# Optimization experiments

Hardware: AMD Instinct MI355X
Metric: run time of the kernel (lower is better)

Reference implementation:

```python
import jax, jax.numpy as jnp
import numpy as np

N = 50000       # nodes per layer
L = 2           # multiplex layers
F_IN = 128
F_OUT = 32
E_L = 800000    # in-layer edges per layer
NEG_SLOPE = 0.2  # LeakyReLU(0.2)


def _merge_edges(edges_per_layer):
    # offset each layer's edges into the global L*N index space
    parts = [edges_per_layer[i] + i * N for i in range(L)]
    all_edges = jnp.concatenate(parts, axis=1)
    dt = all_edges.dtype
    # self loops on every (layer, node)
    self_loops = jnp.tile(jnp.arange(L * N, dtype=dt)[None, :], (2, 1))
    all_edges = jnp.concatenate([all_edges, self_loops], axis=1)
    # interlayer loops: torch.combinations(arange(L), r=2) + flip([0,1])
    pairs = np.array([(i, j) for i in range(L) for j in range(i + 1, L)], dtype=np.int64)
    pairs = np.concatenate([pairs, pairs[::-1, ::-1]], axis=0)
    all_nodes = np.arange(L * N, dtype=np.int64).reshape(L, N)
    src = all_nodes[pairs[:, 0]].reshape(-1)
    trg = all_nodes[pairs[:, 1]].reshape(-1)
    inter = jnp.asarray(np.stack([src, trg], axis=0)).astype(dt)
    return jnp.concatenate([all_edges, inter], axis=1)  # [2, E_total]


def setup_inputs() -> dict:
    key = jax.random.key(0)
    k1, k2, k3, k4, k5 = jax.random.split(key, 5)
    return {
        "x": jax.random.normal(k1, (1, N, F_IN), dtype=jnp.float32),
        "edge_index0": jax.random.randint(k2, (2, E_L), 0, N, dtype=jnp.int32),
        "edge_index1": jax.random.randint(k3, (2, E_L), 0, N, dtype=jnp.int32),
        "W_proj": jax.random.normal(k4, (L * F_OUT, F_IN), dtype=jnp.float32) * 0.05,
        "W_merge": jax.random.normal(k5, (F_OUT, L * F_OUT), dtype=jnp.float32) * 0.05,
        "bias": jnp.zeros((L, F_OUT), dtype=jnp.float32),
    }


def reference(x, edge_index0, edge_index1, W_proj, W_merge, bias):
    # dropout_prob=0 -> dropout is identity (eval-mode semantics)
    B = x.shape[0]
    edges = _merge_edges([edge_index0, edge_index1])
    src, trg = edges[0], edges[1]
    # degree normalization (naming follows original: in_deg from src, out_deg from trg)
    in_deg = 1.0 / jnp.sqrt(jnp.zeros(L * N, x.dtype).at[src].add(1.0))
    out_deg = 1.0 / jnp.sqrt(jnp.zeros(L * N, x.dtype).at[trg].add(1.0))
    # project F_IN -> L*F_OUT, then split features into L chunks concatenated on node dim
    proj = jnp.einsum('bnf,of->bno', x, W_proj)                 # [B, N, L*F_OUT]
    proj = proj.reshape(B, N, L, F_OUT).transpose(0, 2, 1, 3).reshape(B, L * N, F_OUT)
    proj = proj * out_deg[None, :, None]
    lifted = proj[:, src, :]                                    # [B, E, F_OUT] gather
    agg = jnp.zeros((B, L * N, F_OUT), x.dtype).at[:, trg, :].add(lifted)  # scatter_add
    agg = agg * in_deg[None, :, None]
    out = agg.reshape(B, L, N, F_OUT).transpose(0, 2, 1, 3)     # [B, N, L, F_OUT]
    out = jax.nn.leaky_relu(out + bias, NEG_SLOPE)
    return jnp.einsum('bnk,ok->bno', out.reshape(B, N, L * F_OUT), W_merge)  # [B, N, F_OUT]
```

## Files before the change

kernel.cpp:

```cpp
#include <hip/hip_runtime.h>

#define N_NODES 50000
#define F_IN 128
#define F_OUT 32
#define E_L 800000
#define NEG_SLOPE 0.2f
#define LN 100000
#define NE 1600000
#define BSH 6
#define BNODES 64
#define NB 782
#define CAP 2368
#define PBLOCKS 256
#define PCHUNK 6250

__global__ __launch_bounds__(512) void partition_kernel(
    const int* __restrict__ e0, const int* __restrict__ e1,
    int* __restrict__ cur_t, int* __restrict__ cur_s,
    int* __restrict__ trgbuf, unsigned char* __restrict__ srcbuf) {
    __shared__ int hist_t[NB], hist_s[NB], res_t[NB], res_s[NB];
    const int t = threadIdx.x, b = blockIdx.x;
    for (int i = t; i < NB; i += 512) { hist_t[i] = 0; hist_s[i] = 0; }
    __syncthreads();
    const int base = b * PCHUNK;
    for (int i = base + t; i < base + PCHUNK; i += 512) {
        const int l = (i >= E_L) ? 1 : 0;
        const int e = i - l * E_L;
        const int* ei = l ? e1 : e0;
        const int src = ei[e], trg = ei[E_L + e];
        atomicAdd(&hist_t[trg >> BSH], 1);
        atomicAdd(&hist_s[src >> BSH], 1);
    }
    __syncthreads();
    for (int i = t; i < NB; i += 512) {
        res_t[i] = hist_t[i] ? atomicAdd(&cur_t[i], hist_t[i]) : 0;
        res_s[i] = hist_s[i] ? atomicAdd(&cur_s[i], hist_s[i]) : 0;
    }
    __syncthreads();
    for (int i = t; i < NB; i += 512) { hist_t[i] = 0; hist_s[i] = 0; }
    __syncthreads();
    for (int i = base + t; i < base + PCHUNK; i += 512) {
        const int l = (i >= E_L) ? 1 : 0;
        const int e = i - l * E_L;
        const int* ei = l ? e1 : e0;
        const int src = ei[e], trg = ei[E_L + e];
        const int tb = trg >> BSH, sb = src >> BSH;
        const int st = res_t[tb] + atomicAdd(&hist_t[tb], 1);
        const int ss = res_s[sb] + atomicAdd(&hist_s[sb], 1);
        if (st < CAP)
            trgbuf[tb * CAP + st] =
                (((l << 6) | (trg & 63)) << 17) | (src + l * N_NODES);
        if (ss < CAP)
            srcbuf[sb * CAP + ss] = (unsigned char)((l << 6) | (src & 63));
    }
}

__global__ __launch_bounds__(256) void count_kernel(
    const int* __restrict__ cur_t, const int* __restrict__ cur_s,
    const int* __restrict__ trgbuf, const unsigned char* __restrict__ srcbuf,
    int* __restrict__ cnt_trg, int* __restrict__ cnt_src) {
    __shared__ int ht[128], hs[128];
    const int t = threadIdx.x, b = blockIdx.x;
    if (t < 128) { ht[t] = 0; hs[t] = 0; }
    __syncthreads();
    const int ct = min(cur_t[b], CAP), cs = min(cur_s[b], CAP);
    for (int i = t; i < ct; i += 256)
        atomicAdd(&ht[(trgbuf[b * CAP + i] >> 17) & 127], 1);
    for (int i = t; i < cs; i += 256)
        atomicAdd(&hs[srcbuf[b * CAP + i] & 127], 1);
    __syncthreads();
    if (t < 128) {
        const int l = t >> 6, n = b * BNODES + (t & 63);
        if (n < N_NODES) {
            cnt_trg[l * N_NODES + n] = ht[t];
            cnt_src[l * N_NODES + n] = hs[t];
        }
    }
}

__global__ __launch_bounds__(256) void proj_kernel(
    const float* __restrict__ x, const float* __restrict__ Wp,
    const int* __restrict__ cnt_trg, float* __restrict__ scaled) {
    __shared__ float Wtt[64][132];
    __shared__ float xt[8][F_IN];
    const int t = threadIdx.x;
    for (int i = t; i < 64 * F_IN; i += 256) {
        int o = i >> 7, k = i & 127;
        Wtt[o][k] = Wp[i];
    }
    const int lane = t & 63, w = t >> 6;
    const int ntiles = N_NODES / 8;
    for (int tile = blockIdx.x; tile < ntiles; tile += gridDim.x) {
        const int base = tile * 8;
        __syncthreads();
        ((float4*)&xt[0][0])[t] = ((const float4*)(x + (size_t)base * F_IN))[t];
        __syncthreads();
        const int n0 = w, n1 = w + 4;
        float acc0 = 0.f, acc1 = 0.f;
        #pragma unroll
        for (int k = 0; k < F_IN; k += 4) {
            float4 wv = *(const float4*)&Wtt[lane][k];
            float4 x0 = *(const float4*)&xt[n0][k];
            float4 x1 = *(const float4*)&xt[n1][k];
            acc0 += wv.x * x0.x + wv.y * x0.y + wv.z * x0.z + wv.w * x0.w;
            acc1 += wv.x * x1.x + wv.y * x1.y + wv.z * x1.z + wv.w * x1.w;
        }
        const int l = lane >> 5, f = lane & 31;
        {
            const int v = l * N_NODES + base + n0;
            const float od = 1.0f / sqrtf((float)(cnt_trg[v] + 2));
            scaled[(size_t)v * F_OUT + f] = acc0 * od;
        }
        {
            const int v = l * N_NODES + base + n1;
            const float od = 1.0f / sqrtf((float)(cnt_trg[v] + 2));
            scaled[(size_t)v * F_OUT + f] = acc1 * od;
        }
    }
}

__global__ __launch_bounds__(512) void mega_kernel(
    const int* __restrict__ cur_t, const int* __restrict__ trgbuf,
    const int* __restrict__ cnt_trg, const int* __restrict__ cnt_src,
    const float* __restrict__ scaled, const float* __restrict__ Wm,
    const float* __restrict__ bias, float* __restrict__ out) {
    __shared__ int   colx[CAP];
    __shared__ int   rp[128], rdeg[128], cursor[128], sc[128];
    __shared__ float h[BNODES][64];
    __shared__ float Wt[64][32];
    __shared__ float bs[64];
    const int t = threadIdx.x, b = blockIdx.x;
    for (int i = t; i < 2048; i += 512) Wt[i >> 5][i & 31] = Wm[(i & 31) * 64 + (i >> 5)];
    if (t < 64) bs[t] = bias[t];
    int cnt_r = 0;
    if (t < 128) {
        const int l = t >> 6, n = b * BNODES + (t & 63);
        cnt_r = (n < N_NODES) ? cnt_trg[l * N_NODES + n] : 0;
        rdeg[t] = cnt_r; sc[t] = cnt_r;
    }
    __syncthreads();
    for (int off = 1; off < 128; off <<= 1) {
        int add = (t < 128 && t >= off) ? sc[t - off] : 0;
        __syncthreads();
        if (t < 128) sc[t] += add;
        __syncthreads();
    }
    if (t < 128) { rp[t] = sc[t] - cnt_r; cursor[t] = sc[t] - cnt_r; }
    __syncthreads();
    const int total = min(cur_t[b], CAP);
    for (int i = t; i < total; i += 512) {
        const int p = trgbuf[b * CAP + i];
        const int slot = atomicAdd(&cursor[(p >> 17) & 127], 1);
        colx[slot] = p & 0x1FFFF;
    }
    __syncthreads();
    const int grp = t >> 3, f = (t & 7) * 4;
    #pragma unroll
    for (int rr0 = 0; rr0 < 2; ++rr0) {
        const int rr = grp + rr0 * 64;
        const int l = rr >> 6, nl = rr & 63, n = b * BNODES + nl;
        if (n < N_NODES) {
            const int s0 = rp[rr], d = rdeg[rr];
            float4 acc = make_float4(0.f, 0.f, 0.f, 0.f);
            #pragma unroll 4
            for (int i = 0; i < d; ++i) {
                const int u = colx[s0 + i];
                const float4 g = *(const float4*)(scaled + (size_t)u * F_OUT + f);
                acc.x += g.x; acc.y += g.y; acc.z += g.z; acc.w += g.w;
            }
            const int v = l * N_NODES + n, vp = (1 - l) * N_NODES + n;
            const float4 sv = *(const float4*)(scaled + (size_t)v  * F_OUT + f);
            const float4 pv = *(const float4*)(scaled + (size_t)vp * F_OUT + f);
            const float id = rsqrtf((float)(cnt_src[v] + 2));
            float4 hv;
            hv.x = (acc.x + sv.x + pv.x) * id + bs[l * 32 + f + 0];
            hv.y = (acc.y + sv.y + pv.y) * id + bs[l * 32 + f + 1];
            hv.z = (acc.z + sv.z + pv.z) * id + bs[l * 32 + f + 2];
            hv.w = (acc.w + sv.w + pv.w) * id + bs[l * 32 + f + 3];
            hv.x = (hv.x >= 0.f) ? hv.x : NEG_SLOPE * hv.x;
            hv.y = (hv.y >= 0.f) ? hv.y : NEG_SLOPE * hv.y;
            hv.z = (hv.z >= 0.f) ? hv.z : NEG_SLOPE * hv.z;
            hv.w = (hv.w >= 0.f) ? hv.w : NEG_SLOPE * hv.w;
            *(float4*)&h[nl][l * 32 + f] = hv;
        }
    }
    __syncthreads();
    for (int i = t; i < BNODES * 32; i += 512) {
        const int nl = i >> 5, o = i & 31, n = b * BNODES + nl;
        if (n < N_NODES) {
            float acc = 0.f;
            #pragma unroll
            for (int k = 0; k < 64; ++k)
                acc += h[nl][k] * Wt[k][o];
            out[(size_t)n * F_OUT + o] = acc;
        }
    }
}

extern "C" void kernel_launch(void* const* d_in, const int* in_sizes, int n_in,
                              void* d_out, int out_size, void* d_ws, size_t ws_size,
                              hipStream_t stream) {
    const float* x    = (const float*)d_in[0];
    const int*   e0   = (const int*)d_in[1];
    const int*   e1   = (const int*)d_in[2];
    const float* Wp   = (const float*)d_in[3];
    const float* Wm   = (const float*)d_in[4];
    const float* bias = (const float*)d_in[5];
    float* out = (float*)d_out;

    float* scaled = (float*)d_ws;
    unsigned char* srcbuf = (unsigned char*)d_ws;
    int* trgbuf  = (int*)((char*)d_ws + (size_t)LN * F_OUT * sizeof(float));
    int* cur_t   = trgbuf + (size_t)NB * CAP;
    int* cur_s   = cur_t + NB;
    int* cnt_trg = cur_s + NB;
    int* cnt_src = cnt_trg + LN;

    hipMemsetAsync(cur_t, 0, 2 * NB * sizeof(int), stream);

    partition_kernel<<<PBLOCKS, 512, 0, stream>>>(e0, e1, cur_t, cur_s,
                                                  trgbuf, srcbuf);
    count_kernel<<<NB, 256, 0, stream>>>(cur_t, cur_s, trgbuf, srcbuf,
                                         cnt_trg, cnt_src);
    proj_kernel<<<1024, 256, 0, stream>>>(x, Wp, cnt_trg, scaled);
    mega_kernel<<<NB, 512, 0, stream>>>(cur_t, trgbuf, cnt_trg, cnt_src,
                                        scaled, Wm, bias, out);
}
```

Baseline: 189.2 us.

## Cache partition edges in registers and interleave both layers' gathers per node

The partition kernel now runs 512 blocks with half the chunk each, each block confined to one layer. Each thread keeps its edges in registers between the histogram and scatter passes, so the edge arrays are read once instead of twice. The aggregation kernel gives each thread group both layers of one node, interleaving the two neighbor gathers for more memory-level parallelism and sharing the self and interlayer loads. Costs are extra register pressure and divergence when the two layers' degrees differ.

```diff
diff --git a/kernel.cpp b/kernel.cpp
--- a/kernel.cpp
+++ b/kernel.cpp
@@ -11,8 +11,9 @@
 #define BNODES 64
 #define NB 782
 #define CAP 2368
-#define PBLOCKS 256
-#define PCHUNK 6250
+#define PBLOCKS 512
+#define PCHUNK 3125
+#define CEDGE 7
 
 __global__ __launch_bounds__(512) void partition_kernel(
     const int* __restrict__ e0, const int* __restrict__ e1,
@@ -20,16 +21,22 @@
     int* __restrict__ trgbuf, unsigned char* __restrict__ srcbuf) {
     __shared__ int hist_t[NB], hist_s[NB], res_t[NB], res_s[NB];
     const int t = threadIdx.x, b = blockIdx.x;
+    const int l = (b >= PBLOCKS / 2) ? 1 : 0;
+    const int* __restrict__ ei = l ? e1 : e0;
+    const int ebase = b * PCHUNK - l * E_L;
     for (int i = t; i < NB; i += 512) { hist_t[i] = 0; hist_s[i] = 0; }
     __syncthreads();
-    const int base = b * PCHUNK;
-    for (int i = base + t; i < base + PCHUNK; i += 512) {
-        const int l = (i >= E_L) ? 1 : 0;
-        const int e = i - l * E_L;
-        const int* ei = l ? e1 : e0;
-        const int src = ei[e], trg = ei[E_L + e];
-        atomicAdd(&hist_t[trg >> BSH], 1);
-        atomicAdd(&hist_s[src >> BSH], 1);
+    int cs_[CEDGE], ct_[CEDGE];
+    #pragma unroll
+    for (int j = 0; j < CEDGE; ++j) {
+        const int idx = t + j * 512;
+        if (idx < PCHUNK) {
+            const int e = ebase + idx;
+            const int src = ei[e], trg = ei[E_L + e];
+            cs_[j] = src; ct_[j] = trg;
+            atomicAdd(&hist_t[trg >> BSH], 1);
+            atomicAdd(&hist_s[src >> BSH], 1);
+        } else { cs_[j] = -1; ct_[j] = -1; }
     }
     __syncthreads();
     for (int i = t; i < NB; i += 512) {
@@ -39,19 +46,19 @@
     __syncthreads();
     for (int i = t; i < NB; i += 512) { hist_t[i] = 0; hist_s[i] = 0; }
     __syncthreads();
-    for (int i = base + t; i < base + PCHUNK; i += 512) {
-        const int l = (i >= E_L) ? 1 : 0;
-        const int e = i - l * E_L;
-        const int* ei = l ? e1 : e0;
-        const int src = ei[e], trg = ei[E_L + e];
-        const int tb = trg >> BSH, sb = src >> BSH;
-        const int st = res_t[tb] + atomicAdd(&hist_t[tb], 1);
-        const int ss = res_s[sb] + atomicAdd(&hist_s[sb], 1);
-        if (st < CAP)
-            trgbuf[tb * CAP + st] =
-                (((l << 6) | (trg & 63)) << 17) | (src + l * N_NODES);
-        if (ss < CAP)
-            srcbuf[sb * CAP + ss] = (unsigned char)((l << 6) | (src & 63));
+    #pragma unroll
+    for (int j = 0; j < CEDGE; ++j) {
+        if (ct_[j] >= 0) {
+            const int src = cs_[j], trg = ct_[j];
+            const int tb = trg >> BSH, sb = src >> BSH;
+            const int st = res_t[tb] + atomicAdd(&hist_t[tb], 1);
+            const int ss = res_s[sb] + atomicAdd(&hist_s[sb], 1);
+            if (st < CAP)
+                trgbuf[tb * CAP + st] =
+                    (((l << 6) | (trg & 63)) << 17) | (src + l * N_NODES);
+            if (ss < CAP)
+                srcbuf[sb * CAP + ss] = (unsigned char)((l << 6) | (src & 63));
+        }
     }
 }
 
@@ -154,45 +161,61 @@
         colx[slot] = p & 0x1FFFF;
     }
     __syncthreads();
-    const int grp = t >> 3, f = (t & 7) * 4;
-    #pragma unroll
-    for (int rr0 = 0; rr0 < 2; ++rr0) {
-        const int rr = grp + rr0 * 64;
-        const int l = rr >> 6, nl = rr & 63, n = b * BNODES + nl;
-        if (n < N_NODES) {
-            const int s0 = rp[rr], d = rdeg[rr];
-            float4 acc = make_float4(0.f, 0.f, 0.f, 0.f);
-            #pragma unroll 4
-            for (int i = 0; i < d; ++i) {
+    const int nl = t >> 3, f = (t & 7) * 4;
+    const int n = b * BNODES + nl;
+    if (n < N_NODES) {
+        const int s0 = rp[nl],      d0 = rdeg[nl];
+        const int s1 = rp[nl + 64], d1 = rdeg[nl + 64];
+        float4 acc0 = make_float4(0.f, 0.f, 0.f, 0.f);
+        float4 acc1 = make_float4(0.f, 0.f, 0.f, 0.f);
+        const int m = (d0 > d1) ? d0 : d1;
+        #pragma unroll 2
+        for (int i = 0; i < m; ++i) {
+            if (i < d0) {
                 const int u = colx[s0 + i];
                 const float4 g = *(const float4*)(scaled + (size_t)u * F_OUT + f);
-                acc.x += g.x; acc.y += g.y; acc.z += g.z; acc.w += g.w;
+                acc0.x += g.x; acc0.y += g.y; acc0.z += g.z; acc0.w += g.w;
             }
-            const int v = l * N_NODES + n, vp = (1 - l) * N_NODES + n;
-            const float4 sv = *(const float4*)(scaled + (size_t)v  * F_OUT + f);
-            const float4 pv = *(const float4*)(scaled + (size_t)vp * F_OUT + f);
-            const float id = rsqrtf((float)(cnt_src[v] + 2));
-            float4 hv;
-            hv.x = (acc.x + sv.x + pv.x) * id + bs[l * 32 + f + 0];
-            hv.y = (acc.y + sv.y + pv.y) * id + bs[l * 32 + f + 1];
-            hv.z = (acc.z + sv.z + pv.z) * id + bs[l * 32 + f + 2];
-            hv.w = (acc.w + sv.w + pv.w) * id + bs[l * 32 + f + 3];
-            hv.x = (hv.x >= 0.f) ? hv.x : NEG_SLOPE * hv.x;
-            hv.y = (hv.y >= 0.f) ? hv.y : NEG_SLOPE * hv.y;
-            hv.z = (hv.z >= 0.f) ? hv.z : NEG_SLOPE * hv.z;
-            hv.w = (hv.w >= 0.f) ? hv.w : NEG_SLOPE * hv.w;
-            *(float4*)&h[nl][l * 32 + f] = hv;
-        }
+            if (i < d1) {
+                const int u = colx[s1 + i];
+                const float4 g = *(const float4*)(scaled + (size_t)u * F_OUT + f);
+                acc1.x += g.x; acc1.y += g.y; acc1.z += g.z; acc1.w += g.w;
+            }
+        }
+        const int v = n, vp = N_NODES + n;
+        const float4 sv = *(const float4*)(scaled + (size_t)v  * F_OUT + f);
+        const float4 pv = *(const float4*)(scaled + (size_t)vp * F_OUT + f);
+        const float id0 = rsqrtf((float)(cnt_src[v]  + 2));
+        const float id1 = rsqrtf((float)(cnt_src[vp] + 2));
+        float4 h0, h1;
+        h0.x = (acc0.x + sv.x + pv.x) * id0 + bs[f + 0];
+        h0.y = (acc0.y + sv.y + pv.y) * id0 + bs[f + 1];
+        h0.z = (acc0.z + sv.z + pv.z) * id0 + bs[f + 2];
+        h0.w = (acc0.w + sv.w + pv.w) * id0 + bs[f + 3];
+        h1.x = (acc1.x + sv.x + pv.x) * id1 + bs[32 + f + 0];
+        h1.y = (acc1.y + sv.y + pv.y) * id1 + bs[32 + f + 1];
+        h1.z = (acc1.z + sv.z + pv.z) * id1 + bs[32 + f + 2];
+        h1.w = (acc1.w + sv.w + pv.w) * id1 + bs[32 + f + 3];
+        h0.x = (h0.x >= 0.f) ? h0.x : NEG_SLOPE * h0.x;
+        h0.y = (h0.y >= 0.f) ? h0.y : NEG_SLOPE * h0.y;
+        h0.z = (h0.z >= 0.f) ? h0.z : NEG_SLOPE * h0.z;
+        h0.w = (h0.w >= 0.f) ? h0.w : NEG_SLOPE * h0.w;
+        h1.x = (h1.x >= 0.f) ? h1.x : NEG_SLOPE * h1.x;
+        h1.y = (h1.y >= 0.f) ? h1.y : NEG_SLOPE * h1.y;
+        h1.z = (h1.z >= 0.f) ? h1.z : NEG_SLOPE * h1.z;
+        h1.w = (h1.w >= 0.f) ? h1.w : NEG_SLOPE * h1.w;
+        *(float4*)&h[nl][f]      = h0;
+        *(float4*)&h[nl][32 + f] = h1;
     }
     __syncthreads();
     for (int i = t; i < BNODES * 32; i += 512) {
-        const int nl = i >> 5, o = i & 31, n = b * BNODES + nl;
-        if (n < N_NODES) {
+        const int nl2 = i >> 5, o = i & 31, n2 = b * BNODES + nl2;
+        if (n2 < N_NODES) {
             float acc = 0.f;
             #pragma unroll
             for (int k = 0; k < 64; ++k)
-                acc += h[nl][k] * Wt[k][o];
-            out[(size_t)n * F_OUT + o] = acc;
+                acc += h[nl2][k] * Wt[k][o];
+            out[(size_t)n2 * F_OUT + o] = acc;
         }
     }
 }
```

Result: slower. 203.3 us (+7.4%).
